# Performance work log

Hardware: AMD Instinct MI355X
Metric: run time of the kernel (lower is better)

## Reference

```python
import jax, jax.numpy as jnp
import numpy as np

S, D, H, C, A = 2048, 256, 8, 64, 16  # seq_len, node_dim, num_heads, num_channels, num_aux


def setup_inputs() -> dict:
    key = jax.random.key(0)
    ks = jax.random.split(key, 11)
    w = 0.02
    return {
        "nodes": jax.random.normal(ks[0], (S, D), jnp.float32),
        "pos": jax.random.uniform(ks[1], (S, 3), jnp.float32),
        "aux": jax.random.normal(ks[2], (S, A), jnp.float32),
        # eqx.nn.Linear weights are (out_features, in_features); y = W @ x + b
        "W_nodes_kq": jax.random.normal(ks[3], (2 * H * C, D), jnp.float32) * w,
        "b_nodes_kq": jax.random.normal(ks[4], (2 * H * C,), jnp.float32) * w,
        "W_pos_kq": jax.random.normal(ks[5], (2 * H * C, 6), jnp.float32) * w,
        "b_pos_kq": jax.random.normal(ks[6], (2 * H * C,), jnp.float32) * w,
        "W_aux_kq": jax.random.normal(ks[7], (2 * H * C, A), jnp.float32) * w,  # no bias
        "W_val": jax.random.normal(ks[8], (D * H * 3, D), jnp.float32) * w,
        "b_val": jax.random.normal(ks[9], (D * H * 3,), jnp.float32) * w,
        "num_heads": H,
    }


def reference(nodes, pos, aux, W_nodes_kq, b_nodes_kq, W_pos_kq, b_pos_kq,
              W_aux_kq, W_val, b_val, num_heads):
    seq_len = nodes.shape[0]
    # circular positional featurization: [S, 6]
    pos_f = jnp.concatenate([jnp.cos(2 * jnp.pi * pos), jnp.sin(2 * jnp.pi * pos)], axis=-1)
    # values: [S, 3*H, D]
    val = (nodes @ W_val.T + b_val).reshape(seq_len, 3 * num_heads, -1)
    # k/q projections, each reshaped [S, H, 2C] then split into k, q of [S, H, C]
    nodes_k, nodes_q = jnp.split((nodes @ W_nodes_kq.T + b_nodes_kq).reshape(seq_len, num_heads, -1), 2, -1)
    pos_k, pos_q = jnp.split((pos_f @ W_pos_kq.T + b_pos_kq).reshape(seq_len, num_heads, -1), 2, -1)
    aux_k, aux_q = jnp.split((aux @ W_aux_kq.T).reshape(seq_len, num_heads, -1), 2, -1)
    # concat along the HEAD axis -> [S, 3H, C]
    k = jnp.concatenate([nodes_k, pos_k, aux_k], axis=-2)
    q = jnp.concatenate([nodes_q, pos_q, aux_q], axis=-2)
    # all-pairs logits [S, S, 3H]; softmax over the SECOND (query, j) index
    logits = jnp.einsum('ihc,jhc->ijh', k, q)
    att = jax.nn.softmax(logits, axis=-2)
    # weighted sum over j and heads -> [S, D]
    out = jnp.einsum('ijh,jhd->id', att, val)
    return out
```

## Files before the change

kernel.cpp:

```cpp
#include <hip/hip_runtime.h>
#include <math.h>

#define SLEN 2048
#define ND 256
#define NH 24
#define HC 64
#define TWO_PI 6.283185307179586f
#define LOG2E 1.4426950408889634f
#define NT 64

typedef __attribute__((ext_vector_type(8))) short short8;
typedef __attribute__((ext_vector_type(16))) float f32x16;
typedef __attribute__((ext_vector_type(2))) unsigned int uint2e;

static __device__ __forceinline__ unsigned short f2bf(float f) {
    union { float f; unsigned int u; } v; v.f = f;
    unsigned int u = v.u;
    return (unsigned short)((u + 0x7FFFu + ((u >> 16) & 1u)) >> 16);
}
static __device__ __forceinline__ unsigned int pack2(float a, float b) {
    return (unsigned int)f2bf(a) | ((unsigned int)f2bf(b) << 16);
}
static __device__ __forceinline__ unsigned int cvtpk(float lo, float hi) {
    unsigned int r;
    asm("v_cvt_pk_bf16_f32 %0, %1, %2" : "=v"(r) : "v"(lo), "v"(hi));
    return r;
}
static __device__ __forceinline__ float exp2fast(float x) {
    return __builtin_amdgcn_exp2f(x);
}
static __device__ __forceinline__ void gload_lds16(const void* g, void* l) {
    __builtin_amdgcn_global_load_lds(
        (const __attribute__((address_space(1))) void*)(g),
        (__attribute__((address_space(3))) void*)(l), 16, 0, 0);
}

__global__ __launch_bounds__(256) void prep_kernel(
    const float4* __restrict__ Wv, const float4* __restrict__ Wn,
    const float4* __restrict__ nodes, const float* __restrict__ pos,
    uint2* __restrict__ wv_bf, uint2* __restrict__ wn_bf,
    uint2* __restrict__ nodes_bf, float* __restrict__ pos_f)
{
    const unsigned t = blockIdx.x * 256 + threadIdx.x;
    if (t < 589824u) {
        const float4* src; uint2* dst; unsigned id;
        if (t < 393216u)      { src = Wv;    dst = wv_bf;    id = t; }
        else if (t < 458752u) { src = Wn;    dst = wn_bf;    id = t - 393216u; }
        else                  { src = nodes; dst = nodes_bf; id = t - 458752u; }
        float4 v = src[id];
        uint2 u; u.x = pack2(v.x, v.y); u.y = pack2(v.z, v.w);
        dst[id] = u;
    } else {
        const int s = t - 589824u;
        #pragma unroll
        for (int c = 0; c < 3; ++c) {
            float v = pos[s * 3 + c] * TWO_PI;
            pos_f[s * 8 + c] = cosf(v);
            pos_f[s * 8 + 3 + c] = sinf(v);
        }
        pos_f[s * 8 + 6] = 0.f; pos_f[s * 8 + 7] = 0.f;
    }
}

__global__ __launch_bounds__(256) void gemm_kernel(
    const unsigned short* __restrict__ wv_bf, const unsigned short* __restrict__ wn_bf,
    const unsigned short* __restrict__ nodes_bf, const float* __restrict__ bv,
    unsigned short* __restrict__ vt, const float* __restrict__ bn,
    unsigned short* __restrict__ kbf, unsigned short* __restrict__ qbf)
{
    __shared__ __align__(16) char lds[131072];
    const int tid = threadIdx.x;
    const int w = tid >> 6, lane = tid & 63;
    const int l31 = lane & 31, lh = lane >> 5;
    const int bid = blockIdx.x;
    const bool isval = bid < 768;
    int o0, s0;
    const unsigned short *Aptr, *Bptr;
    if (isval) {
        const int wg = ((bid & 7) * 96) + (bid >> 3);
        o0 = (wg >> 4) * 128; s0 = (wg & 15) * 128;
        Aptr = wv_bf + (size_t)o0 * 256; Bptr = nodes_bf + (size_t)s0 * 256;
    } else {
        const int b = bid - 768;
        o0 = (b >> 4) * 128; s0 = (b & 15) * 128;
        Aptr = nodes_bf + (size_t)s0 * 256; Bptr = wn_bf + (size_t)o0 * 256;
    }

    {
        const int rbase = w * 32;
        const int roff = lane >> 5;
        const int slot = l31 * 16;
        #pragma unroll
        for (int i = 0; i < 16; ++i) {
            const int row = rbase + i * 2 + roff;
            const int colb = slot ^ ((row & 31) << 4);
            gload_lds16(Aptr + (((size_t)row) << 8) + (colb >> 1),
                        lds + (rbase + i * 2) * 512);
        }
        #pragma unroll
        for (int i = 0; i < 16; ++i) {
            const int row = rbase + i * 2 + roff;
            const int colb = slot ^ ((row & 31) << 4);
            gload_lds16(Bptr + (((size_t)row) << 8) + (colb >> 1),
                        lds + 65536 + (rbase + i * 2) * 512);
        }
    }
    __syncthreads();

    const int wm = w >> 1, wn = w & 1;
    f32x16 acc[2][2];
    #pragma unroll
    for (int mf = 0; mf < 2; ++mf)
        #pragma unroll
        for (int nf = 0; nf < 2; ++nf)
            #pragma unroll
            for (int r = 0; r < 16; ++r) acc[mf][nf][r] = 0.f;

    const char* Abase = lds;
    const char* Bbase = lds + 65536;
    #pragma unroll
    for (int kk = 0; kk < 16; ++kk) {
        short8 af[2], bq[2];
        #pragma unroll
        for (int mf = 0; mf < 2; ++mf) {
            const int row = wm * 64 + mf * 32 + l31;
            af[mf] = *(const short8*)(Abase + row * 512 +
                     ((kk * 32 + lh * 16) ^ ((row & 31) << 4)));
        }
        #pragma unroll
        for (int nf = 0; nf < 2; ++nf) {
            const int row = wn * 64 + nf * 32 + l31;
            bq[nf] = *(const short8*)(Bbase + row * 512 +
                     ((kk * 32 + lh * 16) ^ ((row & 31) << 4)));
        }
        #pragma unroll
        for (int mf = 0; mf < 2; ++mf)
            #pragma unroll
            for (int nf = 0; nf < 2; ++nf)
                acc[mf][nf] = __builtin_amdgcn_mfma_f32_32x32x16_bf16(
                    af[mf], bq[nf], acc[mf][nf], 0, 0, 0);
    }

    if (isval) {
        #pragma unroll
        for (int mf = 0; mf < 2; ++mf) {
            #pragma unroll
            for (int r = 0; r < 16; ++r) {
                const int o = o0 + wm * 64 + mf * 32 + (r & 3) + 8 * (r >> 2) + 4 * lh;
                const float b = bv[o];
                #pragma unroll
                for (int nf = 0; nf < 2; ++nf) {
                    const int s = s0 + wn * 64 + nf * 32 + l31;
                    vt[(size_t)o * SLEN + s] = f2bf(acc[mf][nf][r] + b);
                }
            }
        }
    } else {
        #pragma unroll
        for (int nf = 0; nf < 2; ++nf) {
            const int o = o0 + wn * 64 + nf * 32 + l31;
            const float bno = bn[o];
            const int h8 = o >> 7, isq = (o >> 6) & 1, c = o & 63;
            unsigned short* dst = isq ? qbf : kbf;
            const float ksc = isq ? 1.0f : LOG2E;
            #pragma unroll
            for (int mf = 0; mf < 2; ++mf) {
                #pragma unroll
                for (int r = 0; r < 16; ++r) {
                    const int s = s0 + wm * 64 + mf * 32 + (r & 3) + 8 * (r >> 2) + 4 * lh;
                    dst[((size_t)h8 * SLEN + s) * HC + c] = f2bf((acc[mf][nf][r] + bno) * ksc);
                }
            }
        }
    }
}

__global__ __launch_bounds__(256) void pa_kernel(
    const float* __restrict__ pos_f, const float* __restrict__ aux,
    const float* __restrict__ bp, const float* __restrict__ Wp,
    const float* __restrict__ Wa,
    unsigned short* __restrict__ kbf, unsigned short* __restrict__ qbf)
{
    __shared__ float wlds[22528];
    const int tid = threadIdx.x;
    for (int i = tid; i < 22528; i += 256)
        wlds[i] = (i < 6144) ? Wp[i] : Wa[i - 6144];
    __syncthreads();

    float bpv[4];
    #pragma unroll
    for (int g = 0; g < 4; ++g) bpv[g] = bp[g * 256 + tid];

    const int s0 = blockIdx.x * 8;
    for (int ss = 0; ss < 8; ++ss) {
        const int s = s0 + ss;
        float pf[6], ax[16];
        #pragma unroll
        for (int d = 0; d < 6; ++d) pf[d] = pos_f[s * 8 + d];
        #pragma unroll
        for (int d = 0; d < 16; ++d) ax[d] = aux[s * 16 + d];
        #pragma unroll
        for (int g = 0; g < 4; ++g) {
            const int op = g * 256 + tid;
            const int hh = op >> 7, iq = (op >> 6) & 1, cc = op & 63;
            unsigned short* dst = iq ? qbf : kbf;
            const float ksc = iq ? 1.0f : LOG2E;
            float vp = bpv[g];
            #pragma unroll
            for (int d = 0; d < 6; ++d) vp += pf[d] * wlds[op * 6 + d];
            float va = 0.f;
            #pragma unroll
            for (int d = 0; d < 16; ++d) va += ax[d] * wlds[6144 + op * 16 + d];
            dst[((size_t)(8 + hh) * SLEN + s) * HC + cc]  = f2bf(vp * ksc);
            dst[((size_t)(16 + hh) * SLEN + s) * HC + cc] = f2bf(va * ksc);
        }
    }
}

__global__ __launch_bounds__(256, 3) void attn_kernel(
    const unsigned short* __restrict__ kbf, const unsigned short* __restrict__ qbf,
    const unsigned short* __restrict__ vt, float* __restrict__ partial)
{
    __shared__ __align__(16) char smem[40960];
    const int BUF = 20480, VOFF = 4096;

    const int tid = threadIdx.x;
    const int w = tid >> 6, lane = tid & 63;
    const int l31 = lane & 31, lh = lane >> 5;
    const int wi = w >> 1, wd = w & 1;
    const int wg = (blockIdx.x & 7) * 96 + (blockIdx.x >> 3);
    const int h = wg >> 5, it = wg & 31;
    const int i0 = it * 64;

    const unsigned short* kh = kbf + (size_t)h * SLEN * HC;
    const unsigned short* qh = qbf + (size_t)h * SLEN * HC;
    const unsigned short* vh = vt + (size_t)h * ND * SLEN;

    short8 kf[4];
    {
        const unsigned short* kp = kh + (size_t)(i0 + wi * 32 + l31) * HC + lh * 8;
        #pragma unroll
        for (int ks = 0; ks < 4; ++ks) kf[ks] = *(const short8*)(kp + ks * 16);
    }

    f32x16 acc[4];
    #pragma unroll
    for (int nf = 0; nf < 4; ++nf)
        #pragma unroll
        for (int r = 0; r < 16; ++r) acc[nf][r] = 0.f;
    float l_run = 0.f;

    const int lrow = lane >> 3;
    const int cu = ((lane & 7) << 4) ^ (lrow << 4);
    const unsigned short* qsrc = qh + (size_t)(w * 8 + lrow) * HC + (cu >> 1);
    const unsigned short* vsrc[4];
    #pragma unroll
    for (int i = 0; i < 4; ++i) {
        const int cc = i * 4 + w;
        const int row = cc * 8 + lrow;
        const int d = row * 2 + (cu >> 6);
        const int j = (cu & 63) >> 1;
        vsrc[i] = vh + (size_t)d * SLEN + j;
    }
    auto stage = [&](int bufo) {
        gload_lds16(qsrc, smem + bufo + w * 1024);
        qsrc += 32 * HC;
        #pragma unroll
        for (int i = 0; i < 4; ++i) {
            gload_lds16(vsrc[i], smem + bufo + VOFF + (i * 4 + w) * 1024);
            vsrc[i] += 32;
        }
    };

    auto softpack = [&](f32x16& S, uint4& p0, uint4& p1) {
        float psum = 0.f;
        #pragma unroll
        for (int r = 0; r < 16; ++r) {
            S[r] = exp2fast(S[r]);
            psum += S[r];
        }
        psum += __shfl_xor(psum, 32);
        l_run += psum;
        uint2e r1 = __builtin_amdgcn_permlane32_swap(cvtpk(S[0], S[1]), cvtpk(S[4], S[5]), false, false);
        uint2e r2 = __builtin_amdgcn_permlane32_swap(cvtpk(S[2], S[3]), cvtpk(S[6], S[7]), false, false);
        uint2e r3 = __builtin_amdgcn_permlane32_swap(cvtpk(S[8], S[9]), cvtpk(S[12], S[13]), false, false);
        uint2e r4 = __builtin_amdgcn_permlane32_swap(cvtpk(S[10], S[11]), cvtpk(S[14], S[15]), false, false);
        p0 = make_uint4(r1[0], r2[0], r1[1], r2[1]);
        p1 = make_uint4(r3[0], r4[0], r3[1], r4[1]);
    };

    stage(0);
    __syncthreads();

    for (int jt = 0; jt < NT; ++jt) {
        const int bo = (jt & 1) * BUF;
        if (jt + 1 < NT) stage(BUF - bo);
        const char* qb = smem + bo;
        const char* vb = smem + bo + VOFF;

        f32x16 S;
        #pragma unroll
        for (int r = 0; r < 16; ++r) S[r] = 0.f;
        const int qsw = (l31 & 7) << 4;
        __builtin_amdgcn_s_setprio(1);
        #pragma unroll
        for (int ks = 0; ks < 4; ++ks) {
            short8 a = *(const short8*)(qb + l31 * 128 + ((ks * 32 + lh * 16) ^ qsw));
            S = __builtin_amdgcn_mfma_f32_32x32x16_bf16(a, kf[ks], S, 0, 0, 0);
        }
        __builtin_amdgcn_s_setprio(0);

        uint4 p0, p1;
        softpack(S, p0, p1);

        __builtin_amdgcn_s_setprio(1);
        #pragma unroll
        for (int ksl = 0; ksl < 2; ++ksl) {
            const short8 pa = *(const short8*)(ksl ? &p1 : &p0);
            #pragma unroll
            for (int nf = 0; nf < 4; ++nf) {
                const int d = wd * 128 + nf * 32 + l31;
                const int row = d >> 1;
                const int colb = (((d & 1) << 6) + ksl * 32 + lh * 16) ^ ((row & 7) << 4);
                short8 vfrag = *(const short8*)(vb + row * 128 + colb);
                acc[nf] = __builtin_amdgcn_mfma_f32_32x32x16_bf16(pa, vfrag, acc[nf], 0, 0, 0);
            }
        }
        __builtin_amdgcn_s_setprio(0);
        __syncthreads();
    }

    float* pb = partial + (size_t)(h / 3) * (SLEN * ND);
    const float invm = 1.0f / l_run;
    float lv[16];
    #pragma unroll
    for (int r = 0; r < 16; ++r)
        lv[r] = __shfl(invm, (r & 3) + 8 * (r >> 2) + 4 * lh);
    #pragma unroll
    for (int nf = 0; nf < 4; ++nf) {
        const int d = wd * 128 + nf * 32 + l31;
        #pragma unroll
        for (int r = 0; r < 16; ++r) {
            const int i = i0 + wi * 32 + (r & 3) + 8 * (r >> 2) + 4 * lh;
            atomicAdd(pb + (size_t)i * ND + d, acc[nf][r] * lv[r]);
        }
    }
}

__global__ __launch_bounds__(256) void reduce_kernel(
    const float4* __restrict__ partial, float4* __restrict__ out)
{
    const size_t id = (size_t)blockIdx.x * 256 + threadIdx.x;
    float4 s = make_float4(0.f, 0.f, 0.f, 0.f);
    #pragma unroll
    for (int g = 0; g < 8; ++g) {
        float4 v = partial[g * (SLEN * ND / 4) + id];
        s.x += v.x; s.y += v.y; s.z += v.z; s.w += v.w;
    }
    out[id] = s;
}

extern "C" void kernel_launch(void* const* d_in, const int* in_sizes, int n_in,
                              void* d_out, int out_size, void* d_ws, size_t ws_size,
                              hipStream_t stream) {
    const float* nodes = (const float*)d_in[0];
    const float* pos   = (const float*)d_in[1];
    const float* aux   = (const float*)d_in[2];
    const float* Wn    = (const float*)d_in[3];
    const float* bn    = (const float*)d_in[4];
    const float* Wp    = (const float*)d_in[5];
    const float* bp    = (const float*)d_in[6];
    const float* Wa    = (const float*)d_in[7];
    const float* Wv    = (const float*)d_in[8];
    const float* bv    = (const float*)d_in[9];
    float* out = (float*)d_out;

    const size_t KQ   = (size_t)SLEN * NH * HC;
    const size_t VT   = (size_t)NH * ND * SLEN;
    const size_t WVBF = (size_t)6144 * ND;
    const size_t WNBF = (size_t)1024 * ND;
    const size_t NDBF = (size_t)SLEN * ND;
    const size_t POSF = (size_t)SLEN * 8;
    const size_t PART = (size_t)8 * SLEN * ND;
    const size_t need = (2 * KQ + VT + WVBF + WNBF + NDBF) * 2 + (POSF + PART) * 4;

    if (ws_size < need) return;

    unsigned short* kbf = (unsigned short*)d_ws;
    unsigned short* qbf = kbf + KQ;
    unsigned short* vt  = qbf + KQ;
    unsigned short* wv_bf = vt + VT;
    unsigned short* wn_bf = wv_bf + WVBF;
    unsigned short* nodes_bf = wn_bf + WNBF;
    float* pos_f   = (float*)(nodes_bf + NDBF);
    float* partial = pos_f + POSF;

    hipMemsetAsync(partial, 0, PART * sizeof(float), stream);
    prep_kernel<<<2312, 256, 0, stream>>>((const float4*)Wv, (const float4*)Wn,
                                          (const float4*)nodes, pos,
                                          (uint2*)wv_bf, (uint2*)wn_bf,
                                          (uint2*)nodes_bf, pos_f);
    gemm_kernel<<<896, 256, 0, stream>>>(wv_bf, wn_bf, nodes_bf, bv, vt, bn, kbf, qbf);
    pa_kernel<<<256, 256, 0, stream>>>(pos_f, aux, bp, Wp, Wa, kbf, qbf);
    attn_kernel<<<768, 256, 0, stream>>>(kbf, qbf, vt, partial);
    reduce_kernel<<<512, 256, 0, stream>>>((const float4*)partial, (float4*)out);
}
```

Baseline: 161.2 us.

## Split attention waves over key tiles instead of output columns, widening j-tiles

The attention kernel now has the two waves of each pair split the j (query) dimension of a 64-wide tile rather than the output D dimension. Each wave computes its own 32x32 logit block once and accumulates over all 256 output columns, so logits and exponentials are no longer computed twice per pair. The row sums from the two waves are combined through shared memory before normalization. In exchange, LDS per block doubles to 80KB and the accumulator registers double, and occupancy is lowered to 2 blocks per SIMD group.

```diff
diff --git a/kernel.cpp b/kernel.cpp
--- a/kernel.cpp
+++ b/kernel.cpp
@@ -7,7 +7,7 @@
 #define HC 64
 #define TWO_PI 6.283185307179586f
 #define LOG2E 1.4426950408889634f
-#define NT 64
+#define NT 32
 
 typedef __attribute__((ext_vector_type(8))) short short8;
 typedef __attribute__((ext_vector_type(16))) float f32x16;
@@ -217,17 +217,17 @@
     }
 }
 
-__global__ __launch_bounds__(256, 3) void attn_kernel(
+__global__ __launch_bounds__(256, 2) void attn_kernel(
     const unsigned short* __restrict__ kbf, const unsigned short* __restrict__ qbf,
     const unsigned short* __restrict__ vt, float* __restrict__ partial)
 {
-    __shared__ __align__(16) char smem[40960];
-    const int BUF = 20480, VOFF = 4096;
+    __shared__ __align__(16) char smem[81920];
+    const int BUF = 40960, VOFF = 8192;
 
     const int tid = threadIdx.x;
     const int w = tid >> 6, lane = tid & 63;
     const int l31 = lane & 31, lh = lane >> 5;
-    const int wi = w >> 1, wd = w & 1;
+    const int wi = w >> 1, wj = w & 1;
     const int wg = (blockIdx.x & 7) * 96 + (blockIdx.x >> 3);
     const int h = wg >> 5, it = wg & 31;
     const int i0 = it * 64;
@@ -243,32 +243,43 @@
         for (int ks = 0; ks < 4; ++ks) kf[ks] = *(const short8*)(kp + ks * 16);
     }
 
-    f32x16 acc[4];
-    #pragma unroll
-    for (int nf = 0; nf < 4; ++nf)
+    f32x16 acc[8];
+    #pragma unroll
+    for (int nf = 0; nf < 8; ++nf)
         #pragma unroll
         for (int r = 0; r < 16; ++r) acc[nf][r] = 0.f;
     float l_run = 0.f;
 
-    const int lrow = lane >> 3;
-    const int cu = ((lane & 7) << 4) ^ (lrow << 4);
-    const unsigned short* qsrc = qh + (size_t)(w * 8 + lrow) * HC + (cu >> 1);
-    const unsigned short* vsrc[4];
-    #pragma unroll
-    for (int i = 0; i < 4; ++i) {
-        const int cc = i * 4 + w;
-        const int row = cc * 8 + lrow;
-        const int d = row * 2 + (cu >> 6);
-        const int j = (cu & 63) >> 1;
-        vsrc[i] = vh + (size_t)d * SLEN + j;
+    const unsigned short* qsrcs[2];
+    {
+        const int qcb = ((lane & 7) << 4) ^ ((lane >> 3) << 4);
+        #pragma unroll
+        for (int i = 0; i < 2; ++i) {
+            const int r = (w * 2 + i) * 8 + (lane >> 3);
+            qsrcs[i] = qh + (size_t)r * HC + (qcb >> 1);
+        }
+    }
+    const unsigned short* vsrcs[8];
+    {
+        const int bb = (lane & 15) << 4;
+        #pragma unroll
+        for (int i = 0; i < 8; ++i) {
+            const int row = (w * 8 + i) * 4 + (lane >> 4);
+            const int d = 2 * row + (bb >> 7);
+            const int jbu = (bb & 127) ^ ((row & 7) << 4);
+            vsrcs[i] = vh + (size_t)d * SLEN + (jbu >> 1);
+        }
     }
     auto stage = [&](int bufo) {
-        gload_lds16(qsrc, smem + bufo + w * 1024);
-        qsrc += 32 * HC;
-        #pragma unroll
-        for (int i = 0; i < 4; ++i) {
-            gload_lds16(vsrc[i], smem + bufo + VOFF + (i * 4 + w) * 1024);
-            vsrc[i] += 32;
+        #pragma unroll
+        for (int i = 0; i < 2; ++i) {
+            gload_lds16(qsrcs[i], smem + bufo + (w * 2 + i) * 1024);
+            qsrcs[i] += 64 * HC;
+        }
+        #pragma unroll
+        for (int i = 0; i < 8; ++i) {
+            gload_lds16(vsrcs[i], smem + bufo + VOFF + (w * 8 + i) * 1024);
+            vsrcs[i] += 64;
         }
     };
 
@@ -301,11 +312,12 @@
         f32x16 S;
         #pragma unroll
         for (int r = 0; r < 16; ++r) S[r] = 0.f;
+        const int qrow = wj * 32 + l31;
         const int qsw = (l31 & 7) << 4;
         __builtin_amdgcn_s_setprio(1);
         #pragma unroll
         for (int ks = 0; ks < 4; ++ks) {
-            short8 a = *(const short8*)(qb + l31 * 128 + ((ks * 32 + lh * 16) ^ qsw));
+            short8 a = *(const short8*)(qb + qrow * 128 + ((ks * 32 + lh * 16) ^ qsw));
             S = __builtin_amdgcn_mfma_f32_32x32x16_bf16(a, kf[ks], S, 0, 0, 0);
         }
         __builtin_amdgcn_s_setprio(0);
@@ -318,11 +330,12 @@
         for (int ksl = 0; ksl < 2; ++ksl) {
             const short8 pa = *(const short8*)(ksl ? &p1 : &p0);
             #pragma unroll
-            for (int nf = 0; nf < 4; ++nf) {
-                const int d = wd * 128 + nf * 32 + l31;
+            for (int nf = 0; nf < 8; ++nf) {
+                const int d = nf * 32 + l31;
                 const int row = d >> 1;
-                const int colb = (((d & 1) << 6) + ksl * 32 + lh * 16) ^ ((row & 7) << 4);
-                short8 vfrag = *(const short8*)(vb + row * 128 + colb);
+                const int bb2 = ((d & 1) << 7) |
+                                ((wj * 64 + ksl * 32 + lh * 16) ^ ((row & 7) << 4));
+                short8 vfrag = *(const short8*)(vb + row * 256 + bb2);
                 acc[nf] = __builtin_amdgcn_mfma_f32_32x32x16_bf16(pa, vfrag, acc[nf], 0, 0, 0);
             }
         }
@@ -330,15 +343,18 @@
         __syncthreads();
     }
 
+    float* lsm = (float*)smem;
+    if (lane < 32) lsm[(wi * 2 + wj) * 32 + l31] = l_run;
+    __syncthreads();
+    const float invl = 1.0f / (lsm[wi * 64 + l31] + lsm[wi * 64 + 32 + l31]);
+    float lv[16];
+    #pragma unroll
+    for (int r = 0; r < 16; ++r)
+        lv[r] = __shfl(invl, (r & 3) + 8 * (r >> 2) + 4 * lh);
     float* pb = partial + (size_t)(h / 3) * (SLEN * ND);
-    const float invm = 1.0f / l_run;
-    float lv[16];
-    #pragma unroll
-    for (int r = 0; r < 16; ++r)
-        lv[r] = __shfl(invm, (r & 3) + 8 * (r >> 2) + 4 * lh);
-    #pragma unroll
-    for (int nf = 0; nf < 4; ++nf) {
-        const int d = wd * 128 + nf * 32 + l31;
+    #pragma unroll
+    for (int nf = 0; nf < 8; ++nf) {
+        const int d = nf * 32 + l31;
         #pragma unroll
         for (int r = 0; r < 16; ++r) {
             const int i = i0 + wi * 32 + (r & 3) + 8 * (r >> 2) + 4 * lh;
```

After: 189.6 us. 17.6% more time.
